# Performance work log

Measured on AMD Instinct MI355X. Metric: run time of the kernel, lower is better.

Reference implementation:

```python
import jax, jax.numpy as jnp
import numpy as np


def setup_inputs() -> dict:
    key = jax.random.key(0)
    ks = jax.random.split(key, 12)
    B, N, M, C = 2, 20000, 4096, 6
    S, K, J = 2, 25, 64          # scales, grid cells (2*2+1)^2, neighbors per cell
    Cin = C + 2                   # xy coords concatenated to features
    Cout = 64
    xyz = jax.random.normal(ks[0], (B, N, 3), dtype=jnp.float32)
    feature = jax.random.normal(ks[1], (B, N, C), dtype=jnp.float32)
    new_xyz = jax.random.normal(ks[2], (B, M, 3), dtype=jnp.float32)
    idx = jax.random.randint(ks[3], (S, B, M, K, J), 0, N, dtype=jnp.int32)
    weight = jax.random.uniform(ks[4], (S, B, M, K, J), dtype=jnp.float32)
    conv_w = jax.random.normal(ks[5], (Cout, Cin, K), dtype=jnp.float32) * 0.05
    conv_b = jnp.zeros((Cout,), dtype=jnp.float32)
    mlp_w0 = jax.random.normal(ks[6], (128, S * Cout), dtype=jnp.float32) * 0.05
    mlp_b0 = jnp.zeros((128,), dtype=jnp.float32)
    mlp_w1 = jax.random.normal(ks[7], (256, 128), dtype=jnp.float32) * 0.05
    mlp_b1 = jnp.zeros((256,), dtype=jnp.float32)
    return {"xyz": xyz, "feature": feature, "new_xyz": new_xyz, "idx": idx,
            "weight": weight, "conv_w": conv_w, "conv_b": conv_b,
            "mlp_w0": mlp_w0, "mlp_b0": mlp_b0, "mlp_w1": mlp_w1, "mlp_b1": mlp_b1}


def reference(xyz, feature, new_xyz, idx, weight, conv_w, conv_b,
              mlp_w0, mlp_b0, mlp_w1, mlp_b1):
    # xyz_feature = cat(xy, feature): (B, N, Cin)
    xf = jnp.concatenate([xyz[:, :, :2], feature], axis=-1)
    center2 = new_xyz[:, :, :2]  # (B, M, 2); remaining channels of center are zero

    def per_scale(idx_s, w_s):
        # idx_s, w_s: (B, M, K, J). Gather neighbor features then bilinear-weight.
        gathered = jax.vmap(lambda f, i: f[i])(xf, idx_s)     # (B, M, K, J, Cin)
        nf = jnp.einsum('bmkj,bmkjc->bmkc', w_s, gathered)    # (B, M, K, Cin)
        nf = nf.at[..., :2].add(-center2[:, :, None, :])      # subtract center (xy only)
        # conv2d with kernel (1, K) over the neighbor axis + ReLU
        out = jnp.einsum('bmkc,ock->bom', nf, conv_w) + conv_b[None, :, None]
        return jax.nn.relu(out)                                # (B, Cout, M)

    outs = [per_scale(idx[s], weight[s]) for s in range(idx.shape[0])]
    x = jnp.concatenate(outs, axis=1)                          # (B, S*Cout, M)
    # SharedMLP: 1x1 convs with ReLU (bn=False)
    x = jax.nn.relu(jnp.einsum('bcm,oc->bom', x, mlp_w0) + mlp_b0[None, :, None])
    x = jax.nn.relu(jnp.einsum('bcm,oc->bom', x, mlp_w1) + mlp_b1[None, :, None])
    result_feature = jnp.transpose(x, (0, 2, 1))               # (B, M, 256)
    return new_xyz, result_feature
```

## Files before the change

### kernel.cpp

```cpp
#include <hip/hip_runtime.h>
#include <hip/hip_bf16.h>

#define B 2
#define N 20000
#define M 4096
#define S 2
#define K 25
#define J 64
#define KJ (K*J)
#define TC 32

#define GPB   64
#define NTH   1024

typedef int   iv4 __attribute__((ext_vector_type(4)));
typedef float fv4 __attribute__((ext_vector_type(4)));

template<int CTRL>
__device__ __forceinline__ float dppadd(float x) {
    return x + __int_as_float(
        __builtin_amdgcn_update_dpp(0, __float_as_int(x), CTRL, 0xF, 0xF, true));
}
__device__ __forceinline__ float red8(float x) {
    x = dppadd<0xB1>(x);
    x = dppadd<0x4E>(x);
    x = dppadd<0x141>(x);
    return x;
}

__global__ __launch_bounds__(256) void prep_kernel(
    const float* __restrict__ xyz, const float* __restrict__ feature,
    const float* __restrict__ new_xyz, const float* __restrict__ conv_w,
    const float* __restrict__ w0, const float* __restrict__ w1,
    __hip_bfloat16* __restrict__ xfh, float* __restrict__ conv_wT,
    float* __restrict__ w0T, float* __restrict__ w1T,
    float* __restrict__ wsum, float* __restrict__ out_newxyz) {
    const int T1 = B * N * 8;
    const int T2 = 208 * 64;
    const int T3 = B * M * 3;
    const int T4 = 128 * 128;
    const int T5 = 128 * 256;
    const int T6 = 128;
    int e = blockIdx.x * blockDim.x + threadIdx.x;
    if (e < T1) {
        int r = e >> 3, t = e & 7;
        int b = r / N, rr = r - b * N;
        int plane = t >> 2, tt = t & 3;
        float v = (t < 2) ? xyz[r * 3 + t] : feature[r * 6 + (t - 2)];
        xfh[((size_t)(b * 2 + plane) * N + rr) * 4 + tt] = __float2bfloat16(v);
    } else if (e < T1 + T2) {
        int e2 = e - T1;
        int i4 = e2 >> 8;
        int rem = e2 & 255;
        int o = rem >> 2, t = rem & 3;
        int i = i4 * 4 + t;
        conv_wT[e2] = (i < 200) ? conv_w[o * 200 + (i & 7) * 25 + (i >> 3)] : 0.f;
    } else if (e < T1 + T2 + T3) {
        int e3 = e - T1 - T2;
        out_newxyz[e3] = new_xyz[e3];
    } else if (e < T1 + T2 + T3 + T4) {
        int e4 = e - T1 - T2 - T3;
        int c = e4 >> 7, o = e4 & 127;
        w0T[e4] = w0[o * 128 + c];
    } else if (e < T1 + T2 + T3 + T4 + T5) {
        int e5 = e - T1 - T2 - T3 - T4;
        int c = e5 >> 8, o = e5 & 255;
        w1T[e5] = w1[o * 128 + c];
    } else if (e < T1 + T2 + T3 + T4 + T5 + T6) {
        int e6 = e - T1 - T2 - T3 - T4 - T5;
        int o = e6 & 63, sel = e6 >> 6;
        float s = 0.f;
        for (int k = 0; k < 25; ++k) s += conv_w[o * 200 + sel * 25 + k];
        wsum[e6] = s;
    }
}

__global__ __launch_bounds__(NTH, 4) void gather_conv_kernel(
    const int* __restrict__ idx, const float* __restrict__ weight,
    const float* __restrict__ new_xyz, const uint2* __restrict__ xfp,
    const float* __restrict__ conv_wT, const float* __restrict__ conv_b,
    const float* __restrict__ wsum,
    float* __restrict__ xmidA, float* __restrict__ xmidB) {
    __shared__ uint2 chunk[N];

    const int bid   = blockIdx.x;
    const int plane = bid & 1;
    const int g0    = (bid >> 1) * GPB;
    const int b     = (g0 >> 12) & (B - 1);
    const uint2* src = xfp + (size_t)(b * 2 + plane) * N;

    const int tid = threadIdx.x;
    for (int r = tid; r < N; r += NTH) chunk[r] = src[r];
    __syncthreads();

    const int team = tid >> 6;
    const int lane = tid & 63;
    const float4* cw4 = (const float4*)conv_wT;
    const int cwo = plane * 64 + lane;

    float acc2[4] = {0.f, 0.f, 0.f, 0.f};

    #pragma unroll 1
    for (int p = 0; p < 4; ++p) {
        const int myk  = p * 8 + (lane >> 3);
        const int mykc = (myk > 24) ? 24 : myk;
        float ar[4][4];

        #pragma unroll
        for (int u = 0; u < 4; ++u) {
            const size_t base = (size_t)(g0 + team * 4 + u) * KJ
                              + (size_t)mykc * J + (lane & 7) * 8;
            const iv4 ia = __builtin_nontemporal_load((const iv4*)(idx + base));
            const iv4 ib = __builtin_nontemporal_load((const iv4*)(idx + base) + 1);
            const fv4 wa = __builtin_nontemporal_load((const fv4*)(weight + base));
            const fv4 wb = __builtin_nontemporal_load((const fv4*)(weight + base) + 1);
            const int   ids[8] = {ia.x, ia.y, ia.z, ia.w, ib.x, ib.y, ib.z, ib.w};
            const float wsv[8] = {wa.x, wa.y, wa.z, wa.w, wb.x, wb.y, wb.z, wb.w};

            float a0 = 0.f, a1 = 0.f, a2 = 0.f, a3 = 0.f;
            #pragma unroll
            for (int j = 0; j < 8; ++j) {
                const uint2 v = chunk[ids[j]];
                const float w = wsv[j];
                a0 = fmaf(w, __uint_as_float(v.x << 16),         a0);
                a1 = fmaf(w, __uint_as_float(v.x & 0xffff0000u), a1);
                a2 = fmaf(w, __uint_as_float(v.y << 16),         a2);
                a3 = fmaf(w, __uint_as_float(v.y & 0xffff0000u), a3);
            }
            ar[u][0] = red8(a0);
            ar[u][1] = red8(a1);
            ar[u][2] = red8(a2);
            ar[u][3] = red8(a3);
        }

        const int nk = (p < 3) ? 8 : 1;
        #pragma unroll
        for (int kk = 0; kk < 8; ++kk) {
            if (kk < nk) {
                const float4 w4 = cw4[(size_t)(p * 8 + kk) * 128 + cwo];
                #pragma unroll
                for (int u = 0; u < 4; ++u) {
                    acc2[u] = fmaf(w4.x, __shfl(ar[u][0], kk * 8, 64), acc2[u]);
                    acc2[u] = fmaf(w4.y, __shfl(ar[u][1], kk * 8, 64), acc2[u]);
                    acc2[u] = fmaf(w4.z, __shfl(ar[u][2], kk * 8, 64), acc2[u]);
                    acc2[u] = fmaf(w4.w, __shfl(ar[u][3], kk * 8, 64), acc2[u]);
                }
            }
        }
    }

    if (plane == 0) {
        const float bo  = conv_b[lane];
        const float wsx = wsum[lane];
        const float wsy = wsum[64 + lane];
        #pragma unroll
        for (int u = 0; u < 4; ++u) {
            const int g = g0 + team * 4 + u;
            const int m = g & (M - 1);
            const int s = g >> 13;
            const float cx = new_xyz[(b * M + m) * 3 + 0];
            const float cy = new_xyz[(b * M + m) * 3 + 1];
            xmidA[((size_t)(b * M + m)) * 128 + s * 64 + lane]
                = acc2[u] + bo - cx * wsx - cy * wsy;
        }
    } else {
        #pragma unroll
        for (int u = 0; u < 4; ++u) {
            const int g = g0 + team * 4 + u;
            const int m = g & (M - 1);
            const int s = g >> 13;
            xmidB[((size_t)(b * M + m)) * 128 + s * 64 + lane] = acc2[u];
        }
    }
}

__global__ __launch_bounds__(256) void mlp0_kernel(
    float* __restrict__ xmidA, const float* __restrict__ xmidB,
    const float* __restrict__ w0T, const float* __restrict__ b0) {
    __shared__ float ws[128 * 128];
    __shared__ float xs[128 * 32];

    int tid = threadIdx.x;
    int col0 = blockIdx.x * TC;

    {
        const float4* w4 = (const float4*)w0T;
        float4* ws4 = (float4*)ws;
        #pragma unroll
        for (int i = 0; i < 16; ++i) ws4[tid + 256 * i] = w4[tid + 256 * i];
    }
    {
        const float4* xa4 = (const float4*)(xmidA + (size_t)col0 * 128);
        const float4* xb4 = (const float4*)(xmidB + (size_t)col0 * 128);
        #pragma unroll
        for (int r = tid; r < 1024; r += 256) {
            int lc = r >> 5, c4 = r & 31;
            float4 va = xa4[lc * 32 + c4];
            float4 vb = xb4[lc * 32 + c4];
            int c = c4 * 4;
            xs[(c + 0) * 32 + lc] = fmaxf(va.x + vb.x, 0.f);
            xs[(c + 1) * 32 + lc] = fmaxf(va.y + vb.y, 0.f);
            xs[(c + 2) * 32 + lc] = fmaxf(va.z + vb.z, 0.f);
            xs[(c + 3) * 32 + lc] = fmaxf(va.w + vb.w, 0.f);
        }
    }
    __syncthreads();

    int og = tid >> 3, cg = tid & 7;
    int o0 = og * 4, lc0 = cg * 4;
    float acc[4][4];
    #pragma unroll
    for (int i = 0; i < 4; ++i) {
        float bv = b0[o0 + i];
        #pragma unroll
        for (int u = 0; u < 4; ++u) acc[i][u] = bv;
    }
    for (int c = 0; c < 128; ++c) {
        float4 xv = *(const float4*)&xs[c * 32 + lc0];
        float4 wv = *(const float4*)&ws[c * 128 + o0];
        acc[0][0] = fmaf(wv.x, xv.x, acc[0][0]);
        acc[0][1] = fmaf(wv.x, xv.y, acc[0][1]);
        acc[0][2] = fmaf(wv.x, xv.z, acc[0][2]);
        acc[0][3] = fmaf(wv.x, xv.w, acc[0][3]);
        acc[1][0] = fmaf(wv.y, xv.x, acc[1][0]);
        acc[1][1] = fmaf(wv.y, xv.y, acc[1][1]);
        acc[1][2] = fmaf(wv.y, xv.z, acc[1][2]);
        acc[1][3] = fmaf(wv.y, xv.w, acc[1][3]);
        acc[2][0] = fmaf(wv.z, xv.x, acc[2][0]);
        acc[2][1] = fmaf(wv.z, xv.y, acc[2][1]);
        acc[2][2] = fmaf(wv.z, xv.z, acc[2][2]);
        acc[2][3] = fmaf(wv.z, xv.w, acc[2][3]);
        acc[3][0] = fmaf(wv.w, xv.x, acc[3][0]);
        acc[3][1] = fmaf(wv.w, xv.y, acc[3][1]);
        acc[3][2] = fmaf(wv.w, xv.z, acc[3][2]);
        acc[3][3] = fmaf(wv.w, xv.w, acc[3][3]);
    }
    #pragma unroll
    for (int u = 0; u < 4; ++u) {
        float4 v = make_float4(fmaxf(acc[0][u], 0.f), fmaxf(acc[1][u], 0.f),
                               fmaxf(acc[2][u], 0.f), fmaxf(acc[3][u], 0.f));
        *(float4*)&xmidA[(size_t)(col0 + lc0 + u) * 128 + o0] = v;
    }
}

__global__ __launch_bounds__(256) void mlp1_kernel(
    const float* __restrict__ xmid,
    const float* __restrict__ w1T, const float* __restrict__ b1,
    float* __restrict__ out_rf) {
    __shared__ float ws[128 * 128];
    __shared__ float xs[128 * 32];

    int tid = threadIdx.x;
    int bx = blockIdx.x;
    int col0 = (bx >> 1) * TC;
    int oH = (bx & 1) * 128;

    {
        for (int i = tid; i < 4096; i += 256) {
            int c = i >> 5, q = i & 31;
            *(float4*)&ws[c * 128 + q * 4] = *(const float4*)&w1T[c * 256 + oH + q * 4];
        }
    }
    {
        const float4* xm4 = (const float4*)(xmid + (size_t)col0 * 128);
        #pragma unroll
        for (int r = tid; r < 1024; r += 256) {
            int lc = r >> 5, c4 = r & 31;
            float4 v = xm4[lc * 32 + c4];
            int c = c4 * 4;
            xs[(c + 0) * 32 + lc] = v.x;
            xs[(c + 1) * 32 + lc] = v.y;
            xs[(c + 2) * 32 + lc] = v.z;
            xs[(c + 3) * 32 + lc] = v.w;
        }
    }
    __syncthreads();

    int og = tid >> 3, cg = tid & 7;
    int o0 = og * 4, lc0 = cg * 4;
    float acc[4][4];
    #pragma unroll
    for (int i = 0; i < 4; ++i) {
        float bv = b1[oH + o0 + i];
        #pragma unroll
        for (int u = 0; u < 4; ++u) acc[i][u] = bv;
    }
    for (int c = 0; c < 128; ++c) {
        float4 xv = *(const float4*)&xs[c * 32 + lc0];
        float4 wv = *(const float4*)&ws[c * 128 + o0];
        acc[0][0] = fmaf(wv.x, xv.x, acc[0][0]);
        acc[0][1] = fmaf(wv.x, xv.y, acc[0][1]);
        acc[0][2] = fmaf(wv.x, xv.z, acc[0][2]);
        acc[0][3] = fmaf(wv.x, xv.w, acc[0][3]);
        acc[1][0] = fmaf(wv.y, xv.x, acc[1][0]);
        acc[1][1] = fmaf(wv.y, xv.y, acc[1][1]);
        acc[1][2] = fmaf(wv.y, xv.z, acc[1][2]);
        acc[1][3] = fmaf(wv.y, xv.w, acc[1][3]);
        acc[2][0] = fmaf(wv.z, xv.x, acc[2][0]);
        acc[2][1] = fmaf(wv.z, xv.y, acc[2][1]);
        acc[2][2] = fmaf(wv.z, xv.z, acc[2][2]);
        acc[2][3] = fmaf(wv.z, xv.w, acc[2][3]);
        acc[3][0] = fmaf(wv.w, xv.x, acc[3][0]);
        acc[3][1] = fmaf(wv.w, xv.y, acc[3][1]);
        acc[3][2] = fmaf(wv.w, xv.z, acc[3][2]);
        acc[3][3] = fmaf(wv.w, xv.w, acc[3][3]);
    }
    #pragma unroll
    for (int u = 0; u < 4; ++u) {
        float4 v = make_float4(fmaxf(acc[0][u], 0.f), fmaxf(acc[1][u], 0.f),
                               fmaxf(acc[2][u], 0.f), fmaxf(acc[3][u], 0.f));
        *(float4*)&out_rf[(size_t)(col0 + lc0 + u) * 256 + oH + o0] = v;
    }
}

extern "C" void kernel_launch(void* const* d_in, const int* in_sizes, int n_in,
                              void* d_out, int out_size, void* d_ws, size_t ws_size,
                              hipStream_t stream) {
    const float* xyz     = (const float*)d_in[0];
    const float* feature = (const float*)d_in[1];
    const float* new_xyz = (const float*)d_in[2];
    const int*   idx     = (const int*)  d_in[3];
    const float* weight  = (const float*)d_in[4];
    const float* conv_w  = (const float*)d_in[5];
    const float* conv_b  = (const float*)d_in[6];
    const float* mlp_w0  = (const float*)d_in[7];
    const float* mlp_b0  = (const float*)d_in[8];
    const float* mlp_w1  = (const float*)d_in[9];
    const float* mlp_b1  = (const float*)d_in[10];

    float* out    = (float*)d_out;
    float* out_rf = out + (size_t)B * M * 3;

    float* wsf = (float*)d_ws;
    __hip_bfloat16* xfh = (__hip_bfloat16*)wsf;
    float* conv_wT = wsf + 160000;
    float* xmidA   = conv_wT + 13312;
    float* w0T     = xmidA + 1048576;
    float* w1T     = w0T + 16384;
    float* wsum    = w1T + 32768;
    float* xmidB   = out_rf;

    {
        int total = 320000 + 13312 + 24576 + 16384 + 32768 + 128;
        int blocks = (total + 255) / 256;
        prep_kernel<<<blocks, 256, 0, stream>>>(xyz, feature, new_xyz, conv_w,
                                                mlp_w0, mlp_w1,
                                                xfh, conv_wT, w0T, w1T, wsum, out);
    }
    {
        int blocks = 2 * (S * B * M) / GPB;
        gather_conv_kernel<<<blocks, NTH, 0, stream>>>(idx, weight, new_xyz,
                                                       (const uint2*)xfh,
                                                       conv_wT, conv_b, wsum,
                                                       xmidA, xmidB);
    }
    {
        mlp0_kernel<<<(B * M) / TC, 256, 0, stream>>>(xmidA, xmidB, w0T, mlp_b0);
    }
    {
        mlp1_kernel<<<2 * (B * M) / TC, 256, 0, stream>>>(xmidA, w1T, mlp_b1, out_rf);
    }
}
```

Baseline: 324.9 us.

## Software-pipeline gather loads, double groups per block, fuse both MLP kernels

The gather-conv kernel now handles 128 groups per block, halving how often the 20000-entry LDS table is refilled. Its index/weight loads are explicitly software-pipelined two units ahead of the LDS gather-and-reduce work, with the conv accumulation unrolled per k-group. The two MLP kernels are merged into one that keeps the hidden activations in shared memory, removing a global round trip and a launch. xmidB moves into workspace because the fused kernel writes out_rf while its inputs may still be live, at the cost of more register pressure in the gather kernel.

```diff
diff --git a/kernel.cpp b/kernel.cpp
--- a/kernel.cpp
+++ b/kernel.cpp
@@ -10,7 +10,7 @@
 #define KJ (K*J)
 #define TC 32
 
-#define GPB   64
+#define GPB   128
 #define NTH   1024
 
 typedef int   iv4 __attribute__((ext_vector_type(4)));
@@ -75,6 +75,51 @@
     }
 }
 
+struct UD { iv4 ia, ib; fv4 wa, wb; };
+
+__device__ __forceinline__ UD loadu(const int* __restrict__ idx,
+                                    const float* __restrict__ weight,
+                                    size_t base) {
+    UD d;
+    d.ia = __builtin_nontemporal_load((const iv4*)(idx + base));
+    d.ib = __builtin_nontemporal_load((const iv4*)(idx + base) + 1);
+    d.wa = __builtin_nontemporal_load((const fv4*)(weight + base));
+    d.wb = __builtin_nontemporal_load((const fv4*)(weight + base) + 1);
+    return d;
+}
+
+__device__ __forceinline__ void procu(const UD& d, const uint2* chunk, float* ar) {
+    const int   ids[8] = {d.ia.x, d.ia.y, d.ia.z, d.ia.w, d.ib.x, d.ib.y, d.ib.z, d.ib.w};
+    const float wsv[8] = {d.wa.x, d.wa.y, d.wa.z, d.wa.w, d.wb.x, d.wb.y, d.wb.z, d.wb.w};
+    float a0 = 0.f, a1 = 0.f, a2 = 0.f, a3 = 0.f;
+    #pragma unroll
+    for (int j = 0; j < 8; ++j) {
+        const uint2 v = chunk[ids[j]];
+        const float w = wsv[j];
+        a0 = fmaf(w, __uint_as_float(v.x << 16),         a0);
+        a1 = fmaf(w, __uint_as_float(v.x & 0xffff0000u), a1);
+        a2 = fmaf(w, __uint_as_float(v.y << 16),         a2);
+        a3 = fmaf(w, __uint_as_float(v.y & 0xffff0000u), a3);
+    }
+    ar[0] = red8(a0); ar[1] = red8(a1); ar[2] = red8(a2); ar[3] = red8(a3);
+}
+
+template<int NK>
+__device__ __forceinline__ void convp(const float4* __restrict__ wp,
+                                      const float (*ar)[4], float* acc2) {
+    #pragma unroll
+    for (int kk = 0; kk < NK; ++kk) {
+        const float4 w4 = wp[(size_t)kk * 128];
+        #pragma unroll
+        for (int u = 0; u < 4; ++u) {
+            acc2[u] = fmaf(w4.x, __shfl(ar[u][0], kk * 8, 64), acc2[u]);
+            acc2[u] = fmaf(w4.y, __shfl(ar[u][1], kk * 8, 64), acc2[u]);
+            acc2[u] = fmaf(w4.z, __shfl(ar[u][2], kk * 8, 64), acc2[u]);
+            acc2[u] = fmaf(w4.w, __shfl(ar[u][3], kk * 8, 64), acc2[u]);
+        }
+    }
+}
+
 __global__ __launch_bounds__(NTH, 4) void gather_conv_kernel(
     const int* __restrict__ idx, const float* __restrict__ weight,
     const float* __restrict__ new_xyz, const uint2* __restrict__ xfp,
@@ -97,124 +142,73 @@
     const int lane = tid & 63;
     const float4* cw4 = (const float4*)conv_wT;
     const int cwo = plane * 64 + lane;
-
-    float acc2[4] = {0.f, 0.f, 0.f, 0.f};
+    const int lg  = lane >> 3;
+    const size_t joff = (size_t)((lane & 7) * 8);
+
+    const float bo  = conv_b[lane];
+    const float wsx = wsum[lane];
+    const float wsy = wsum[64 + lane];
+
+    const size_t mkJ0 = (size_t)(lg) * J;
+    const size_t mkJ1 = (size_t)(8 + lg) * J;
+    const size_t mkJ2 = (size_t)(16 + lg) * J;
+    const size_t mkJ3 = (size_t)24 * J;
 
     #pragma unroll 1
-    for (int p = 0; p < 4; ++p) {
-        const int myk  = p * 8 + (lane >> 3);
-        const int mykc = (myk > 24) ? 24 : myk;
+    for (int set = 0; set < 2; ++set) {
+        const int gbase = g0 + team * 8 + set * 4;
+        const size_t gb = (size_t)gbase * KJ + joff;
+        float acc2[4] = {0.f, 0.f, 0.f, 0.f};
         float ar[4][4];
 
-        #pragma unroll
-        for (int u = 0; u < 4; ++u) {
-            const size_t base = (size_t)(g0 + team * 4 + u) * KJ
-                              + (size_t)mykc * J + (lane & 7) * 8;
-            const iv4 ia = __builtin_nontemporal_load((const iv4*)(idx + base));
-            const iv4 ib = __builtin_nontemporal_load((const iv4*)(idx + base) + 1);
-            const fv4 wa = __builtin_nontemporal_load((const fv4*)(weight + base));
-            const fv4 wb = __builtin_nontemporal_load((const fv4*)(weight + base) + 1);
-            const int   ids[8] = {ia.x, ia.y, ia.z, ia.w, ib.x, ib.y, ib.z, ib.w};
-            const float wsv[8] = {wa.x, wa.y, wa.z, wa.w, wb.x, wb.y, wb.z, wb.w};
-
-            float a0 = 0.f, a1 = 0.f, a2 = 0.f, a3 = 0.f;
+        UD d0  = loadu(idx, weight, gb + 0 * KJ + mkJ0);
+        UD d1  = loadu(idx, weight, gb + 1 * KJ + mkJ0);
+        UD d2  = loadu(idx, weight, gb + 2 * KJ + mkJ0);  procu(d0,  chunk, ar[0]);
+        UD d3  = loadu(idx, weight, gb + 3 * KJ + mkJ0);  procu(d1,  chunk, ar[1]);
+        UD d4  = loadu(idx, weight, gb + 0 * KJ + mkJ1);  procu(d2,  chunk, ar[2]);
+        UD d5  = loadu(idx, weight, gb + 1 * KJ + mkJ1);  procu(d3,  chunk, ar[3]);
+        convp<8>(cw4 + (size_t)0 * 1024 + cwo, ar, acc2);
+        UD d6  = loadu(idx, weight, gb + 2 * KJ + mkJ1);  procu(d4,  chunk, ar[0]);
+        UD d7  = loadu(idx, weight, gb + 3 * KJ + mkJ1);  procu(d5,  chunk, ar[1]);
+        UD d8  = loadu(idx, weight, gb + 0 * KJ + mkJ2);  procu(d6,  chunk, ar[2]);
+        UD d9  = loadu(idx, weight, gb + 1 * KJ + mkJ2);  procu(d7,  chunk, ar[3]);
+        convp<8>(cw4 + (size_t)1 * 1024 + cwo, ar, acc2);
+        UD d10 = loadu(idx, weight, gb + 2 * KJ + mkJ2);  procu(d8,  chunk, ar[0]);
+        UD d11 = loadu(idx, weight, gb + 3 * KJ + mkJ2);  procu(d9,  chunk, ar[1]);
+        UD d12 = loadu(idx, weight, gb + 0 * KJ + mkJ3);  procu(d10, chunk, ar[2]);
+        UD d13 = loadu(idx, weight, gb + 1 * KJ + mkJ3);  procu(d11, chunk, ar[3]);
+        convp<8>(cw4 + (size_t)2 * 1024 + cwo, ar, acc2);
+        UD d14 = loadu(idx, weight, gb + 2 * KJ + mkJ3);  procu(d12, chunk, ar[0]);
+        UD d15 = loadu(idx, weight, gb + 3 * KJ + mkJ3);  procu(d13, chunk, ar[1]);
+        procu(d14, chunk, ar[2]);
+        procu(d15, chunk, ar[3]);
+        convp<1>(cw4 + (size_t)3 * 1024 + cwo, ar, acc2);
+
+        if (plane == 0) {
             #pragma unroll
-            for (int j = 0; j < 8; ++j) {
-                const uint2 v = chunk[ids[j]];
-                const float w = wsv[j];
-                a0 = fmaf(w, __uint_as_float(v.x << 16),         a0);
-                a1 = fmaf(w, __uint_as_float(v.x & 0xffff0000u), a1);
-                a2 = fmaf(w, __uint_as_float(v.y << 16),         a2);
-                a3 = fmaf(w, __uint_as_float(v.y & 0xffff0000u), a3);
+            for (int u = 0; u < 4; ++u) {
+                const int g = gbase + u;
+                const int m = g & (M - 1);
+                const int s = g >> 13;
+                const float cx = new_xyz[(b * M + m) * 3 + 0];
+                const float cy = new_xyz[(b * M + m) * 3 + 1];
+                xmidA[((size_t)(b * M + m)) * 128 + s * 64 + lane]
+                    = acc2[u] + bo - cx * wsx - cy * wsy;
             }
-            ar[u][0] = red8(a0);
-            ar[u][1] = red8(a1);
-            ar[u][2] = red8(a2);
-            ar[u][3] = red8(a3);
-        }
-
-        const int nk = (p < 3) ? 8 : 1;
-        #pragma unroll
-        for (int kk = 0; kk < 8; ++kk) {
-            if (kk < nk) {
-                const float4 w4 = cw4[(size_t)(p * 8 + kk) * 128 + cwo];
-                #pragma unroll
-                for (int u = 0; u < 4; ++u) {
-                    acc2[u] = fmaf(w4.x, __shfl(ar[u][0], kk * 8, 64), acc2[u]);
-                    acc2[u] = fmaf(w4.y, __shfl(ar[u][1], kk * 8, 64), acc2[u]);
-                    acc2[u] = fmaf(w4.z, __shfl(ar[u][2], kk * 8, 64), acc2[u]);
-                    acc2[u] = fmaf(w4.w, __shfl(ar[u][3], kk * 8, 64), acc2[u]);
-                }
+        } else {
+            #pragma unroll
+            for (int u = 0; u < 4; ++u) {
+                const int g = gbase + u;
+                const int m = g & (M - 1);
+                const int s = g >> 13;
+                xmidB[((size_t)(b * M + m)) * 128 + s * 64 + lane] = acc2[u];
             }
         }
     }
-
-    if (plane == 0) {
-        const float bo  = conv_b[lane];
-        const float wsx = wsum[lane];
-        const float wsy = wsum[64 + lane];
-        #pragma unroll
-        for (int u = 0; u < 4; ++u) {
-            const int g = g0 + team * 4 + u;
-            const int m = g & (M - 1);
-            const int s = g >> 13;
-            const float cx = new_xyz[(b * M + m) * 3 + 0];
-            const float cy = new_xyz[(b * M + m) * 3 + 1];
-            xmidA[((size_t)(b * M + m)) * 128 + s * 64 + lane]
-                = acc2[u] + bo - cx * wsx - cy * wsy;
-        }
-    } else {
-        #pragma unroll
-        for (int u = 0; u < 4; ++u) {
-            const int g = g0 + team * 4 + u;
-            const int m = g & (M - 1);
-            const int s = g >> 13;
-            xmidB[((size_t)(b * M + m)) * 128 + s * 64 + lane] = acc2[u];
-        }
-    }
-}
-
-__global__ __launch_bounds__(256) void mlp0_kernel(
-    float* __restrict__ xmidA, const float* __restrict__ xmidB,
-    const float* __restrict__ w0T, const float* __restrict__ b0) {
-    __shared__ float ws[128 * 128];
-    __shared__ float xs[128 * 32];
-
-    int tid = threadIdx.x;
-    int col0 = blockIdx.x * TC;
-
-    {
-        const float4* w4 = (const float4*)w0T;
-        float4* ws4 = (float4*)ws;
-        #pragma unroll
-        for (int i = 0; i < 16; ++i) ws4[tid + 256 * i] = w4[tid + 256 * i];
-    }
-    {
-        const float4* xa4 = (const float4*)(xmidA + (size_t)col0 * 128);
-        const float4* xb4 = (const float4*)(xmidB + (size_t)col0 * 128);
-        #pragma unroll
-        for (int r = tid; r < 1024; r += 256) {
-            int lc = r >> 5, c4 = r & 31;
-            float4 va = xa4[lc * 32 + c4];
-            float4 vb = xb4[lc * 32 + c4];
-            int c = c4 * 4;
-            xs[(c + 0) * 32 + lc] = fmaxf(va.x + vb.x, 0.f);
-            xs[(c + 1) * 32 + lc] = fmaxf(va.y + vb.y, 0.f);
-            xs[(c + 2) * 32 + lc] = fmaxf(va.z + vb.z, 0.f);
-            xs[(c + 3) * 32 + lc] = fmaxf(va.w + vb.w, 0.f);
-        }
-    }
-    __syncthreads();
-
-    int og = tid >> 3, cg = tid & 7;
-    int o0 = og * 4, lc0 = cg * 4;
-    float acc[4][4];
-    #pragma unroll
-    for (int i = 0; i < 4; ++i) {
-        float bv = b0[o0 + i];
-        #pragma unroll
-        for (int u = 0; u < 4; ++u) acc[i][u] = bv;
-    }
+}
+
+__device__ __forceinline__ void gemm_tile(const float* xs, const float* ws,
+                                          int o0, int lc0, float acc[4][4]) {
     for (int c = 0; c < 128; ++c) {
         float4 xv = *(const float4*)&xs[c * 32 + lc0];
         float4 wv = *(const float4*)&ws[c * 128 + o0];
@@ -235,81 +229,98 @@
         acc[3][2] = fmaf(wv.w, xv.z, acc[3][2]);
         acc[3][3] = fmaf(wv.w, xv.w, acc[3][3]);
     }
-    #pragma unroll
-    for (int u = 0; u < 4; ++u) {
-        float4 v = make_float4(fmaxf(acc[0][u], 0.f), fmaxf(acc[1][u], 0.f),
-                               fmaxf(acc[2][u], 0.f), fmaxf(acc[3][u], 0.f));
-        *(float4*)&xmidA[(size_t)(col0 + lc0 + u) * 128 + o0] = v;
-    }
-}
-
-__global__ __launch_bounds__(256) void mlp1_kernel(
-    const float* __restrict__ xmid,
+}
+
+__global__ __launch_bounds__(256) void mlp01_kernel(
+    const float* __restrict__ xmidA, const float* __restrict__ xmidB,
+    const float* __restrict__ w0T, const float* __restrict__ b0,
     const float* __restrict__ w1T, const float* __restrict__ b1,
     float* __restrict__ out_rf) {
     __shared__ float ws[128 * 128];
     __shared__ float xs[128 * 32];
 
     int tid = threadIdx.x;
-    int bx = blockIdx.x;
-    int col0 = (bx >> 1) * TC;
-    int oH = (bx & 1) * 128;
-
-    {
-        for (int i = tid; i < 4096; i += 256) {
-            int c = i >> 5, q = i & 31;
-            *(float4*)&ws[c * 128 + q * 4] = *(const float4*)&w1T[c * 256 + oH + q * 4];
-        }
-    }
-    {
-        const float4* xm4 = (const float4*)(xmid + (size_t)col0 * 128);
+    int col0 = blockIdx.x * TC;
+    int og = tid >> 3, cg = tid & 7;
+    int o0 = og * 4, lc0 = cg * 4;
+
+    {
+        const float4* w4 = (const float4*)w0T;
+        float4* ws4 = (float4*)ws;
+        #pragma unroll
+        for (int i = 0; i < 16; ++i) ws4[tid + 256 * i] = w4[tid + 256 * i];
+    }
+    {
+        const float4* xa4 = (const float4*)(xmidA + (size_t)col0 * 128);
+        const float4* xb4 = (const float4*)(xmidB + (size_t)col0 * 128);
         #pragma unroll
         for (int r = tid; r < 1024; r += 256) {
             int lc = r >> 5, c4 = r & 31;
-            float4 v = xm4[lc * 32 + c4];
+            float4 va = xa4[lc * 32 + c4];
+            float4 vb = xb4[lc * 32 + c4];
             int c = c4 * 4;
-            xs[(c + 0) * 32 + lc] = v.x;
-            xs[(c + 1) * 32 + lc] = v.y;
-            xs[(c + 2) * 32 + lc] = v.z;
-            xs[(c + 3) * 32 + lc] = v.w;
+            xs[(c + 0) * 32 + lc] = fmaxf(va.x + vb.x, 0.f);
+            xs[(c + 1) * 32 + lc] = fmaxf(va.y + vb.y, 0.f);
+            xs[(c + 2) * 32 + lc] = fmaxf(va.z + vb.z, 0.f);
+            xs[(c + 3) * 32 + lc] = fmaxf(va.w + vb.w, 0.f);
         }
     }
     __syncthreads();
 
-    int og = tid >> 3, cg = tid & 7;
-    int o0 = og * 4, lc0 = cg * 4;
     float acc[4][4];
     #pragma unroll
     for (int i = 0; i < 4; ++i) {
-        float bv = b1[oH + o0 + i];
+        float bv = b0[o0 + i];
         #pragma unroll
         for (int u = 0; u < 4; ++u) acc[i][u] = bv;
     }
-    for (int c = 0; c < 128; ++c) {
-        float4 xv = *(const float4*)&xs[c * 32 + lc0];
-        float4 wv = *(const float4*)&ws[c * 128 + o0];
-        acc[0][0] = fmaf(wv.x, xv.x, acc[0][0]);
-        acc[0][1] = fmaf(wv.x, xv.y, acc[0][1]);
-        acc[0][2] = fmaf(wv.x, xv.z, acc[0][2]);
-        acc[0][3] = fmaf(wv.x, xv.w, acc[0][3]);
-        acc[1][0] = fmaf(wv.y, xv.x, acc[1][0]);
-        acc[1][1] = fmaf(wv.y, xv.y, acc[1][1]);
-        acc[1][2] = fmaf(wv.y, xv.z, acc[1][2]);
-        acc[1][3] = fmaf(wv.y, xv.w, acc[1][3]);
-        acc[2][0] = fmaf(wv.z, xv.x, acc[2][0]);
-        acc[2][1] = fmaf(wv.z, xv.y, acc[2][1]);
-        acc[2][2] = fmaf(wv.z, xv.z, acc[2][2]);
-        acc[2][3] = fmaf(wv.z, xv.w, acc[2][3]);
-        acc[3][0] = fmaf(wv.w, xv.x, acc[3][0]);
-        acc[3][1] = fmaf(wv.w, xv.y, acc[3][1]);
-        acc[3][2] = fmaf(wv.w, xv.z, acc[3][2]);
-        acc[3][3] = fmaf(wv.w, xv.w, acc[3][3]);
-    }
+    gemm_tile(xs, ws, o0, lc0, acc);
+    __syncthreads();
+
+    #pragma unroll
+    for (int i = 0; i < 4; ++i)
+        #pragma unroll
+        for (int u = 0; u < 4; ++u)
+            xs[(o0 + i) * 32 + lc0 + u] = fmaxf(acc[i][u], 0.f);
+    for (int i = tid; i < 4096; i += 256) {
+        int c = i >> 5, q = i & 31;
+        *(float4*)&ws[c * 128 + q * 4] = *(const float4*)&w1T[c * 256 + q * 4];
+    }
+    __syncthreads();
+
+    #pragma unroll
+    for (int i = 0; i < 4; ++i) {
+        float bv = b1[o0 + i];
+        #pragma unroll
+        for (int u = 0; u < 4; ++u) acc[i][u] = bv;
+    }
+    gemm_tile(xs, ws, o0, lc0, acc);
     #pragma unroll
     for (int u = 0; u < 4; ++u) {
         float4 v = make_float4(fmaxf(acc[0][u], 0.f), fmaxf(acc[1][u], 0.f),
                                fmaxf(acc[2][u], 0.f), fmaxf(acc[3][u], 0.f));
-        *(float4*)&out_rf[(size_t)(col0 + lc0 + u) * 256 + oH + o0] = v;
+        *(float4*)&out_rf[(size_t)(col0 + lc0 + u) * 256 + o0] = v;
+    }
+    __syncthreads();
+
+    for (int i = tid; i < 4096; i += 256) {
+        int c = i >> 5, q = i & 31;
+        *(float4*)&ws[c * 128 + q * 4] = *(const float4*)&w1T[c * 256 + 128 + q * 4];
+    }
+    __syncthreads();
+
+    #pragma unroll
+    for (int i = 0; i < 4; ++i) {
+        float bv = b1[128 + o0 + i];
+        #pragma unroll
+        for (int u = 0; u < 4; ++u) acc[i][u] = bv;
+    }
+    gemm_tile(xs, ws, o0, lc0, acc);
+    #pragma unroll
+    for (int u = 0; u < 4; ++u) {
+        float4 v = make_float4(fmaxf(acc[0][u], 0.f), fmaxf(acc[1][u], 0.f),
+                               fmaxf(acc[2][u], 0.f), fmaxf(acc[3][u], 0.f));
+        *(float4*)&out_rf[(size_t)(col0 + lc0 + u) * 256 + 128 + o0] = v;
     }
 }
 
@@ -338,7 +349,7 @@
     float* w0T     = xmidA + 1048576;
     float* w1T     = w0T + 16384;
     float* wsum    = w1T + 32768;
-    float* xmidB   = out_rf;
+    float* xmidB   = wsum + 128;
 
     {
         int total = 320000 + 13312 + 24576 + 16384 + 32768 + 128;
@@ -355,9 +366,8 @@
                                                        xmidA, xmidB);
     }
     {
-        mlp0_kernel<<<(B * M) / TC, 256, 0, stream>>>(xmidA, xmidB, w0T, mlp_b0);
-    }
-    {
-        mlp1_kernel<<<2 * (B * M) / TC, 256, 0, stream>>>(xmidA, w1T, mlp_b1, out_rf);
-    }
-}
+        mlp01_kernel<<<(B * M) / TC, 256, 0, stream>>>(xmidA, xmidB,
+                                                       w0T, mlp_b0,
+                                                       w1T, mlp_b1, out_rf);
+    }
+}
```

Result: slower. 363.4 us (+11.9%).
